# Optimization experiments

Hardware: AMD Instinct MI355X
Metric: run time of the kernel (lower is better)

## Reference

```python
import jax, jax.numpy as jnp
import numpy as np

N, E, G = 50000, 400000, 64          # nodes, edges, graphs in batch
IN_DIM, OUT_DIM = 64, 128
N_ETYPES, N_STEPS = 4, 8


def setup_inputs() -> dict:
    key = jax.random.key(0)
    ks = jax.random.split(key, 13)
    s = 1.0 / np.sqrt(OUT_DIM)
    u = lambda k, shp: jax.random.uniform(k, shp, jnp.float32, -s, s)
    return {
        "node_features": jax.random.normal(ks[0], (N, IN_DIM), jnp.float32),
        "src": jax.random.randint(ks[1], (E,), 0, N),
        "dst": jax.random.randint(ks[2], (E,), 0, N),
        "etype": jax.random.randint(ks[3], (E,), 0, N_ETYPES),
        "graph_ids": jax.random.randint(ks[4], (N,), 0, G),
        "Ws": u(ks[5], (N_ETYPES, OUT_DIM, OUT_DIM)),   # per-edge-type linear
        "bs": u(ks[6], (N_ETYPES, OUT_DIM)),
        "W_ih": u(ks[7], (3 * OUT_DIM, OUT_DIM)),        # GRUCell (r,z,n order)
        "W_hh": u(ks[8], (3 * OUT_DIM, OUT_DIM)),
        "b_ih": u(ks[9], (3 * OUT_DIM,)),
        "b_hh": u(ks[10], (3 * OUT_DIM,)),
        "W_cls": u(ks[11], (1, OUT_DIM + IN_DIM)),
        "b_cls": u(ks[12], (1,)),
    }


def _gru_cell(x, h, W_ih, W_hh, b_ih, b_hh):
    gi = x @ W_ih.T + b_ih
    gh = h @ W_hh.T + b_hh
    ir, iz, i_n = jnp.split(gi, 3, axis=-1)
    hr, hz, h_n = jnp.split(gh, 3, axis=-1)
    r = jax.nn.sigmoid(ir + hr)
    z = jax.nn.sigmoid(iz + hz)
    n = jnp.tanh(i_n + r * h_n)
    return (1.0 - z) * n + z * h


def reference(node_features, src, dst, etype, graph_ids,
              Ws, bs, W_ih, W_hh, b_ih, b_hh, W_cls, b_cls):
    # pad input features to OUT_DIM (GGNN.forward zero_pad)
    h = jnp.concatenate(
        [node_features, jnp.zeros((N, OUT_DIM - IN_DIM), node_features.dtype)], -1)

    def step(h, _):
        # per-edge-type linear transform of all node states: (T, N, D)
        Wh = jnp.einsum('nd,tkd->tnk', h, Ws) + bs[:, None, :]
        msg = Wh[etype, src]                                  # (E, D) gather
        a = jax.ops.segment_sum(msg, dst, num_segments=N)     # scatter-add
        return _gru_cell(a, h, W_ih, W_hh, b_ih, b_hh), None

    h, _ = jax.lax.scan(step, h, None, length=N_STEPS)

    hcat = jnp.concatenate([h, node_features], -1)            # (N, OUT+IN)
    feats = jax.ops.segment_sum(hcat, graph_ids, num_segments=G)  # sum readout
    return jax.nn.sigmoid(feats @ W_cls.T + b_cls)            # (G, 1)
```

## Files before the change

### kernel.cpp

```cpp
#include <hip/hip_runtime.h>
#include <hip/hip_bf16.h>
#include <math.h>


#define NN 50000
#define NE 400000
#define NG 64
#define IND 64
#define OD 128
#define NN4 (NN * 4)
#define LDO 768
#define RC 8

typedef _Float16 f16x8 __attribute__((ext_vector_type(8)));
typedef _Float16 f16x4 __attribute__((ext_vector_type(4)));
typedef _Float16 f16x2 __attribute__((ext_vector_type(2)));
typedef float f32x4 __attribute__((ext_vector_type(4)));

__device__ inline unsigned short f2h(float x) {
    _Float16 hv = (_Float16)x;
    unsigned short u;
    __builtin_memcpy(&u, &hv, 2);
    return u;
}

__global__ void k_cvt(const float* __restrict__ s, unsigned short* __restrict__ d, int n) {
    int i = blockIdx.x * 256 + threadIdx.x;
    if (i < n) d[i] = f2h(s[i]);
}

__global__ void k_init_h(const float* __restrict__ nf, float* __restrict__ h,
                         unsigned short* __restrict__ hb) {
    int i = blockIdx.x * 256 + threadIdx.x;
    if (i >= NN * OD) return;
    int n = i >> 7, d = i & 127;
    float v = (d < IND) ? nf[n * IND + d] : 0.f;
    h[i] = v;
    hb[i] = f2h(v);
}

__global__ void k_count(const int* __restrict__ dst, const int* __restrict__ et,
                        int* __restrict__ deg4) {
    int e = blockIdx.x * 256 + threadIdx.x;
    if (e < NE) atomicAdd(&deg4[dst[e] * 4 + et[e]], 1);
}

__global__ void k_scan1(const int* __restrict__ deg, int* __restrict__ rowp,
                        int* __restrict__ bsum, int n) {
    __shared__ int buf[1024];
    int tid = threadIdx.x;
    int i = blockIdx.x * 1024 + tid;
    int v = (i < n) ? deg[i] : 0;
    buf[tid] = v;
    __syncthreads();
    for (int off = 1; off < 1024; off <<= 1) {
        int t = (tid >= off) ? buf[tid - off] : 0;
        __syncthreads();
        buf[tid] += t;
        __syncthreads();
    }
    if (i < n) rowp[i + 1] = buf[tid];
    if (tid == 1023) bsum[blockIdx.x] = buf[tid];
}

__global__ void k_scan2(int* __restrict__ bsum, int nb) {
    __shared__ int buf[256];
    int tid = threadIdx.x;
    int v = (tid < nb) ? bsum[tid] : 0;
    buf[tid] = v;
    __syncthreads();
    for (int off = 1; off < 256; off <<= 1) {
        int t = (tid >= off) ? buf[tid - off] : 0;
        __syncthreads();
        buf[tid] += t;
        __syncthreads();
    }
    if (tid < nb) bsum[tid] = buf[tid] - v;
}

__global__ void k_scan3(const int* __restrict__ deg, const int* __restrict__ bsum,
                        int* __restrict__ rowp, int* __restrict__ cursor, int n) {
    int i = blockIdx.x * 256 + threadIdx.x;
    if (i >= n) return;
    int incl = rowp[i + 1] + bsum[i >> 10];
    rowp[i + 1] = incl;
    cursor[i] = incl - deg[i];
    if (i == 0) rowp[0] = 0;
}

__global__ void k_fill(const int* __restrict__ src, const int* __restrict__ dst,
                       const int* __restrict__ et, int* __restrict__ cursor,
                       int* __restrict__ esrc) {
    int e = blockIdx.x * 256 + threadIdx.x;
    if (e < NE) {
        int pos = atomicAdd(&cursor[dst[e] * 4 + et[e]], 1);
        esrc[pos] = src[e];
    }
}

__global__ void k_gcount(const int* __restrict__ gid, int* __restrict__ gdeg) {
    __shared__ int c[NG];
    int tid = threadIdx.x;
    if (tid < NG) c[tid] = 0;
    __syncthreads();
    int n = blockIdx.x * 1024 + tid;
    if (n < NN) atomicAdd(&c[gid[n]], 1);
    __syncthreads();
    if (tid < NG && c[tid] > 0) atomicAdd(&gdeg[tid], c[tid]);
}

__global__ void k_gscan(const int* __restrict__ gdeg, int* __restrict__ growp,
                        int* __restrict__ gcur) {
    __shared__ int buf[NG];
    int tid = threadIdx.x;
    int v = gdeg[tid];
    buf[tid] = v;
    __syncthreads();
    for (int off = 1; off < NG; off <<= 1) {
        int t = (tid >= off) ? buf[tid - off] : 0;
        __syncthreads();
        buf[tid] += t;
        __syncthreads();
    }
    growp[tid + 1] = buf[tid];
    gcur[tid] = buf[tid] - v;
    if (tid == 0) growp[0] = 0;
}

__global__ void k_gfill(const int* __restrict__ gid, int* __restrict__ gcur,
                        int* __restrict__ nlist) {
    __shared__ int lcnt[NG];
    __shared__ int lbase[NG];
    int tid = threadIdx.x;
    if (tid < NG) lcnt[tid] = 0;
    __syncthreads();
    int n = blockIdx.x * 1024 + tid;
    int g = -1, rank = 0;
    if (n < NN) { g = gid[n]; rank = atomicAdd(&lcnt[g], 1); }
    __syncthreads();
    if (tid < NG && lcnt[tid] > 0) lbase[tid] = atomicAdd(&gcur[tid], lcnt[tid]);
    __syncthreads();
    if (n < NN) nlist[lbase[g] + rank] = n;
}

__global__ __launch_bounds__(256) void k_agg_gemm(
    const unsigned short* __restrict__ hb,
    const int* __restrict__ rowp4, const int* __restrict__ esrc,
    const int* __restrict__ deg4,
    const unsigned short* __restrict__ Wsb,
    const float* __restrict__ bs,
    unsigned short* __restrict__ ab) {
    __shared__ unsigned short Ss[128 * 136];
    __shared__ float Bsb[512];

    const int tid = threadIdx.x;
    const int m0 = blockIdx.x * 128;

    Bsb[tid] = bs[tid];
    Bsb[tid + 256] = bs[tid + 256];

    const int r = tid >> 1;
    const int hsel = tid & 1;
    const int n = m0 + r;

    const int lane = tid & 63;
    const int w = tid >> 6;
    const int lr = lane & 15;
    const int q = lane >> 4;

    f32x4 acc[2][8];
#pragma unroll
    for (int mt = 0; mt < 2; ++mt)
#pragma unroll
        for (int nt = 0; nt < 8; ++nt) acc[mt][nt] = (f32x4){0.f, 0.f, 0.f, 0.f};

    for (int t = 0; t < 4; ++t) {
        float sacc[64];
#pragma unroll
        for (int j = 0; j < 64; ++j) sacc[j] = 0.f;
        if (n < NN) {
            int beg = rowp4[n * 4 + t], end = rowp4[n * 4 + t + 1];
            for (int i = beg; i < end; ++i) {
                const f16x8* row8 = (const f16x8*)&hb[(size_t)esrc[i] * 128 + hsel * 64];
#pragma unroll
                for (int jj = 0; jj < 8; ++jj) {
                    f16x8 v = row8[jj];
#pragma unroll
                    for (int k = 0; k < 8; ++k) sacc[jj * 8 + k] += (float)v[k];
                }
            }
        }
        __syncthreads();
#pragma unroll
        for (int jj = 0; jj < 8; ++jj) {
            f16x8 hv;
#pragma unroll
            for (int k = 0; k < 8; ++k) hv[k] = (_Float16)sacc[jj * 8 + k];
            *(f16x8*)&Ss[r * 136 + hsel * 64 + jj * 8] = hv;
        }
        __syncthreads();

        const unsigned short* Wt = Wsb + t * 16384;
#pragma unroll
        for (int ks = 0; ks < 4; ++ks) {
            f16x8 af[2];
#pragma unroll
            for (int mt = 0; mt < 2; ++mt)
                af[mt] = *(const f16x8*)&Ss[(w * 32 + mt * 16 + lr) * 136 + ks * 32 + q * 8];
#pragma unroll
            for (int nt = 0; nt < 8; ++nt) {
                f16x8 bf = *(const f16x8*)&Wt[(nt * 16 + lr) * 128 + ks * 32 + q * 8];
#pragma unroll
                for (int mt = 0; mt < 2; ++mt)
                    acc[mt][nt] = __builtin_amdgcn_mfma_f32_16x16x32_f16(
                        af[mt], bf, acc[mt][nt], 0, 0, 0);
            }
        }
    }

#pragma unroll
    for (int mt = 0; mt < 2; ++mt) {
        int rowbase = m0 + w * 32 + mt * 16 + q * 4;
#pragma unroll
        for (int rr = 0; rr < 4; ++rr) {
            int n2 = rowbase + rr;
            if (n2 < NN) {
                int4 c = *(const int4*)&deg4[n2 * 4];
                unsigned short* arow = ab + (size_t)n2 * 128;
#pragma unroll
                for (int nt = 0; nt < 8; ++nt) {
                    int col = nt * 16 + lr;
                    float v = acc[mt][nt][rr]
                            + c.x * Bsb[col] + c.y * Bsb[128 + col]
                            + c.z * Bsb[256 + col] + c.w * Bsb[384 + col];
                    arow[col] = f2h(v);
                }
            }
        }
    }
}

__global__ __launch_bounds__(256) void k_gates_gemm(
    const unsigned short* __restrict__ Aab, const unsigned short* __restrict__ Ahb,
    int M,
    const unsigned short* __restrict__ Wih, const unsigned short* __restrict__ Whh,
    const float* __restrict__ bih, const float* __restrict__ bhh,
    unsigned short* __restrict__ C) {
    __shared__ unsigned short As[128 * 136];
    __shared__ unsigned short Bs[128 * 136];

    const int g = blockIdx.y;
    const unsigned short* Ab = (g < 3) ? Aab : Ahb;
    const unsigned short* W  = (g < 3) ? (Wih + (size_t)g * 16384)
                                       : (Whh + (size_t)(g - 3) * 16384);
    const float* bias = (g < 3) ? (bih + g * 128) : (bhh + (g - 3) * 128);
    const int colbase = g * 128;
    const int m0 = blockIdx.x * 128;
    const int tid = threadIdx.x;

    const uint4* A4 = (const uint4*)Ab;
    const uint4* W4 = (const uint4*)W;

#pragma unroll
    for (int i = tid; i < 2048; i += 256) {
        int row = i >> 4, qq = i & 15;
        int nn = m0 + row;
        uint4 va = (nn < M) ? A4[(size_t)nn * 16 + qq] : make_uint4(0u, 0u, 0u, 0u);
        *(uint4*)&As[row * 136 + qq * 8] = va;
        *(uint4*)&Bs[row * 136 + qq * 8] = W4[(size_t)row * 16 + qq];
    }
    __syncthreads();

    const int lane = tid & 63;
    const int w = tid >> 6;
    const int lr = lane & 15;
    const int q = lane >> 4;

    float bv[8];
#pragma unroll
    for (int nt = 0; nt < 8; ++nt) bv[nt] = bias[nt * 16 + lr];

    f32x4 acc[2][8];
#pragma unroll
    for (int mt = 0; mt < 2; ++mt)
#pragma unroll
        for (int nt = 0; nt < 8; ++nt) acc[mt][nt] = (f32x4){0.f, 0.f, 0.f, 0.f};

#pragma unroll
    for (int ks = 0; ks < 4; ++ks) {
        f16x8 af[2];
#pragma unroll
        for (int mt = 0; mt < 2; ++mt)
            af[mt] = *(const f16x8*)&As[(w * 32 + mt * 16 + lr) * 136 + ks * 32 + q * 8];
        f16x8 bfr[8];
#pragma unroll
        for (int nt = 0; nt < 8; ++nt)
            bfr[nt] = *(const f16x8*)&Bs[(nt * 16 + lr) * 136 + ks * 32 + q * 8];
#pragma unroll
        for (int mt = 0; mt < 2; ++mt)
#pragma unroll
            for (int nt = 0; nt < 8; ++nt)
                acc[mt][nt] = __builtin_amdgcn_mfma_f32_16x16x32_f16(
                    af[mt], bfr[nt], acc[mt][nt], 0, 0, 0);
    }

#pragma unroll
    for (int mt = 0; mt < 2; ++mt) {
        int rowbase = m0 + w * 32 + mt * 16 + q * 4;
#pragma unroll
        for (int rr = 0; rr < 4; ++rr) {
            int nn = rowbase + rr;
            if (nn < M) {
                unsigned short* crow = C + (size_t)nn * LDO + colbase;
#pragma unroll
                for (int nt = 0; nt < 8; ++nt)
                    crow[nt * 16 + lr] = f2h(acc[mt][nt][rr] + bv[nt]);
            }
        }
    }
}

__global__ void k_gru(const unsigned short* __restrict__ O, float* __restrict__ h,
                      unsigned short* __restrict__ hb) {
    int i = blockIdx.x * 256 + threadIdx.x;
    if (i >= NN * 64) return;
    int n = i >> 6, p = (i & 63) * 2;
    const unsigned short* r = O + (size_t)n * LDO;
    f16x2 ir = *(const f16x2*)&r[p];
    f16x2 iz = *(const f16x2*)&r[128 + p];
    f16x2 in_ = *(const f16x2*)&r[256 + p];
    f16x2 hr = *(const f16x2*)&r[384 + p];
    f16x2 hz = *(const f16x2*)&r[512 + p];
    f16x2 hn = *(const f16x2*)&r[640 + p];
    float2 hv = *(const float2*)&h[(size_t)n * OD + p];
    float2 nh;
    {
        float rg = 1.f / (1.f + __expf(-((float)ir[0] + (float)hr[0])));
        float zg = 1.f / (1.f + __expf(-((float)iz[0] + (float)hz[0])));
        float ng = tanhf((float)in_[0] + rg * (float)hn[0]);
        nh.x = (1.f - zg) * ng + zg * hv.x;
        rg = 1.f / (1.f + __expf(-((float)ir[1] + (float)hr[1])));
        zg = 1.f / (1.f + __expf(-((float)iz[1] + (float)hz[1])));
        ng = tanhf((float)in_[1] + rg * (float)hn[1]);
        nh.y = (1.f - zg) * ng + zg * hv.y;
    }
    *(float2*)&h[(size_t)n * OD + p] = nh;
    f16x2 hb2; hb2[0] = (_Float16)nh.x; hb2[1] = (_Float16)nh.y;
    *(f16x2*)&hb[(size_t)n * OD + p] = hb2;
}

__global__ void k_readout(const float* __restrict__ h, const float* __restrict__ nf,
                          const int* __restrict__ nlist, const int* __restrict__ growp,
                          float* __restrict__ partial) {
    int g = blockIdx.x >> 3, c = blockIdx.x & (RC - 1);
    int d = threadIdx.x;
    int s = growp[g], e = growp[g + 1], len = e - s;
    int i0 = s + (int)((long long)len * c / RC);
    int i1 = s + (int)((long long)len * (c + 1) / RC);
    float acc = 0.f;
    for (int i = i0; i < i1; ++i) {
        int n = nlist[i];
        acc += (d < OD) ? h[(size_t)n * OD + d] : nf[(size_t)n * IND + (d - OD)];
    }
    partial[(size_t)blockIdx.x * 192 + d] = acc;
}

__global__ void k_reduce(const float* __restrict__ partial, float* __restrict__ feats) {
    int i = blockIdx.x * 256 + threadIdx.x;
    if (i >= NG * 192) return;
    int g = i / 192, d = i % 192;
    float s = 0.f;
    for (int c = 0; c < RC; ++c) s += partial[(size_t)(g * RC + c) * 192 + d];
    feats[i] = s;
}

__global__ void k_final(const float* __restrict__ feats, const float* __restrict__ W_cls,
                        const float* __restrict__ b_cls, float* __restrict__ out) {
    int g = threadIdx.x;
    if (g >= NG) return;
    float acc = b_cls[0];
    for (int d = 0; d < 192; ++d) acc += feats[g * 192 + d] * W_cls[d];
    out[g] = 1.f / (1.f + __expf(-acc));
}

extern "C" void kernel_launch(void* const* d_in, const int* in_sizes, int n_in,
                              void* d_out, int out_size, void* d_ws, size_t ws_size,
                              hipStream_t stream) {
    const float* nf    = (const float*)d_in[0];
    const int*   src   = (const int*)d_in[1];
    const int*   dst   = (const int*)d_in[2];
    const int*   et    = (const int*)d_in[3];
    const int*   gid   = (const int*)d_in[4];
    const float* Ws    = (const float*)d_in[5];
    const float* bs    = (const float*)d_in[6];
    const float* W_ih  = (const float*)d_in[7];
    const float* W_hh  = (const float*)d_in[8];
    const float* b_ih  = (const float*)d_in[9];
    const float* b_hh  = (const float*)d_in[10];
    const float* W_cls = (const float*)d_in[11];
    const float* b_cls = (const float*)d_in[12];
    float* out = (float*)d_out;

    char* ws = (char*)d_ws;
    size_t off = 0;
    auto alloc = [&](size_t bytes) -> void* {
        off = (off + 255) & ~(size_t)255;
        void* p = ws + off;
        off += bytes;
        return p;
    };
    float*          h    = (float*)alloc((size_t)NN * OD * 4);
    unsigned short* O    = (unsigned short*)alloc((size_t)NN * LDO * 2);
    unsigned short* hb   = (unsigned short*)alloc((size_t)NN * OD * 2);
    unsigned short* ab   = (unsigned short*)alloc((size_t)NN * OD * 2);
    int*   deg4    = (int*)alloc((size_t)NN4 * 4);
    int*   rowp4   = (int*)alloc((size_t)(NN4 + 1) * 4);
    int*   cursor4 = (int*)alloc((size_t)NN4 * 4);
    int*   esrc    = (int*)alloc((size_t)NE * 4);
    int*   bsum    = (int*)alloc(256 * 4);
    int*   gdeg    = (int*)alloc(NG * 4);
    int*   growp   = (int*)alloc((NG + 1) * 4);
    int*   gcur    = (int*)alloc(NG * 4);
    int*   nlist   = (int*)alloc((size_t)NN * 4);
    float* feats   = (float*)alloc((size_t)NG * 192 * 4);
    unsigned short* wsb  = (unsigned short*)alloc((size_t)4 * 16384 * 2);
    unsigned short* wihb = (unsigned short*)alloc((size_t)3 * 16384 * 2);
    unsigned short* whhb = (unsigned short*)alloc((size_t)3 * 16384 * 2);
    (void)ws_size; (void)in_sizes; (void)n_in; (void)out_size;

    float* partial = (float*)O;

    hipMemsetAsync(deg4, 0, (size_t)NN4 * 4, stream);
    hipMemsetAsync(gdeg, 0, NG * 4, stream);

    k_cvt<<<(4 * 16384 + 255) / 256, 256, 0, stream>>>(Ws, wsb, 4 * 16384);
    k_cvt<<<(3 * 16384 + 255) / 256, 256, 0, stream>>>(W_ih, wihb, 3 * 16384);
    k_cvt<<<(3 * 16384 + 255) / 256, 256, 0, stream>>>(W_hh, whhb, 3 * 16384);

    k_init_h<<<(NN * OD + 255) / 256, 256, 0, stream>>>(nf, h, hb);

    k_count<<<(NE + 255) / 256, 256, 0, stream>>>(dst, et, deg4);
    const int nb4 = (NN4 + 1023) / 1024;
    k_scan1<<<nb4, 1024, 0, stream>>>(deg4, rowp4, bsum, NN4);
    k_scan2<<<1, 256, 0, stream>>>(bsum, nb4);
    k_scan3<<<(NN4 + 255) / 256, 256, 0, stream>>>(deg4, bsum, rowp4, cursor4, NN4);
    k_fill<<<(NE + 255) / 256, 256, 0, stream>>>(src, dst, et, cursor4, esrc);

    const int nbn = (NN + 1023) / 1024;
    k_gcount<<<nbn, 1024, 0, stream>>>(gid, gdeg);
    k_gscan<<<1, NG, 0, stream>>>(gdeg, growp, gcur);
    k_gfill<<<nbn, 1024, 0, stream>>>(gid, gcur, nlist);

    const int mt = (NN + 127) / 128;
    for (int s = 0; s < 8; ++s) {
        k_agg_gemm<<<mt, 256, 0, stream>>>(hb, rowp4, esrc, deg4, wsb, bs, ab);
        k_gates_gemm<<<dim3(mt, 6), 256, 0, stream>>>(ab, hb, NN, wihb, whhb,
                                                      b_ih, b_hh, O);
        k_gru<<<(NN * 64 + 255) / 256, 256, 0, stream>>>(O, h, hb);
    }

    k_readout<<<NG * RC, 192, 0, stream>>>(h, nf, nlist, growp, partial);
    k_reduce<<<(NG * 192 + 255) / 256, 256, 0, stream>>>(partial, feats);
    k_final<<<1, 64, 0, stream>>>(feats, W_cls, b_cls, out);
}
```

Baseline: 1.165 ms.

## Fuse gate GEMMs with GRU update and interleave a/h into one buffer

```diff
diff --git a/kernel.cpp b/kernel.cpp
--- a/kernel.cpp
+++ b/kernel.cpp
@@ -9,7 +9,6 @@
 #define IND 64
 #define OD 128
 #define NN4 (NN * 4)
-#define LDO 768
 #define RC 8
 
 typedef _Float16 f16x8 __attribute__((ext_vector_type(8)));
@@ -29,14 +28,37 @@
     if (i < n) d[i] = f2h(s[i]);
 }
 
+__global__ void k_pack(const float* __restrict__ Wih, const float* __restrict__ Whh,
+                       const float* __restrict__ bih, const float* __restrict__ bhh,
+                       unsigned short* __restrict__ Wpk, float* __restrict__ bpk) {
+    int i = blockIdx.x * 256 + threadIdx.x;
+    if (i < 65536) {
+        int o = i >> 8, k = i & 255;
+        float v = (k < 128) ? Wih[o * 128 + k] : Whh[o * 128 + (k - 128)];
+        Wpk[i] = f2h(v);
+    } else if (i < 98304) {
+        int j = i - 65536;
+        int o = j >> 7, k = j & 127;
+        float v = (o < 128) ? Wih[(256 + o) * 128 + k] : Whh[(256 + (o - 128)) * 128 + k];
+        Wpk[i] = f2h(v);
+    }
+    if (i < 512) {
+        float b;
+        if (i < 256) b = bih[i] + bhh[i];
+        else if (i < 384) b = bih[i];
+        else b = bhh[i - 128];
+        bpk[i] = b;
+    }
+}
+
 __global__ void k_init_h(const float* __restrict__ nf, float* __restrict__ h,
-                         unsigned short* __restrict__ hb) {
+                         unsigned short* __restrict__ hx) {
     int i = blockIdx.x * 256 + threadIdx.x;
     if (i >= NN * OD) return;
     int n = i >> 7, d = i & 127;
     float v = (d < IND) ? nf[n * IND + d] : 0.f;
     h[i] = v;
-    hb[i] = f2h(v);
+    hx[(size_t)n * 256 + 128 + d] = f2h(v);
 }
 
 __global__ void k_count(const int* __restrict__ dst, const int* __restrict__ et,
@@ -144,23 +166,23 @@
 }
 
 __global__ __launch_bounds__(256) void k_agg_gemm(
-    const unsigned short* __restrict__ hb,
+    const unsigned short* __restrict__ hx,
     const int* __restrict__ rowp4, const int* __restrict__ esrc,
     const int* __restrict__ deg4,
     const unsigned short* __restrict__ Wsb,
     const float* __restrict__ bs,
-    unsigned short* __restrict__ ab) {
-    __shared__ unsigned short Ss[128 * 136];
+    unsigned short* __restrict__ hxw) {
+    __shared__ unsigned short Ss[64 * 136];
     __shared__ float Bsb[512];
 
     const int tid = threadIdx.x;
-    const int m0 = blockIdx.x * 128;
+    const int m0 = blockIdx.x * 64;
 
     Bsb[tid] = bs[tid];
     Bsb[tid + 256] = bs[tid + 256];
 
-    const int r = tid >> 1;
-    const int hsel = tid & 1;
+    const int r = tid >> 2;
+    const int hsel = tid & 3;
     const int n = m0 + r;
 
     const int lane = tid & 63;
@@ -168,22 +190,21 @@
     const int lr = lane & 15;
     const int q = lane >> 4;
 
-    f32x4 acc[2][8];
-#pragma unroll
-    for (int mt = 0; mt < 2; ++mt)
-#pragma unroll
-        for (int nt = 0; nt < 8; ++nt) acc[mt][nt] = (f32x4){0.f, 0.f, 0.f, 0.f};
+    f32x4 acc[8];
+#pragma unroll
+    for (int nt = 0; nt < 8; ++nt) acc[nt] = (f32x4){0.f, 0.f, 0.f, 0.f};
 
     for (int t = 0; t < 4; ++t) {
-        float sacc[64];
-#pragma unroll
-        for (int j = 0; j < 64; ++j) sacc[j] = 0.f;
+        float sacc[32];
+#pragma unroll
+        for (int j = 0; j < 32; ++j) sacc[j] = 0.f;
         if (n < NN) {
             int beg = rowp4[n * 4 + t], end = rowp4[n * 4 + t + 1];
             for (int i = beg; i < end; ++i) {
-                const f16x8* row8 = (const f16x8*)&hb[(size_t)esrc[i] * 128 + hsel * 64];
-#pragma unroll
-                for (int jj = 0; jj < 8; ++jj) {
+                const f16x8* row8 =
+                    (const f16x8*)&hx[(size_t)esrc[i] * 256 + 128 + hsel * 32];
+#pragma unroll
+                for (int jj = 0; jj < 4; ++jj) {
                     f16x8 v = row8[jj];
 #pragma unroll
                     for (int k = 0; k < 8; ++k) sacc[jj * 8 + k] += (float)v[k];
@@ -192,82 +213,68 @@
         }
         __syncthreads();
 #pragma unroll
-        for (int jj = 0; jj < 8; ++jj) {
+        for (int jj = 0; jj < 4; ++jj) {
             f16x8 hv;
 #pragma unroll
             for (int k = 0; k < 8; ++k) hv[k] = (_Float16)sacc[jj * 8 + k];
-            *(f16x8*)&Ss[r * 136 + hsel * 64 + jj * 8] = hv;
+            *(f16x8*)&Ss[r * 136 + hsel * 32 + jj * 8] = hv;
         }
         __syncthreads();
 
         const unsigned short* Wt = Wsb + t * 16384;
 #pragma unroll
         for (int ks = 0; ks < 4; ++ks) {
-            f16x8 af[2];
-#pragma unroll
-            for (int mt = 0; mt < 2; ++mt)
-                af[mt] = *(const f16x8*)&Ss[(w * 32 + mt * 16 + lr) * 136 + ks * 32 + q * 8];
+            f16x8 af = *(const f16x8*)&Ss[(w * 16 + lr) * 136 + ks * 32 + q * 8];
 #pragma unroll
             for (int nt = 0; nt < 8; ++nt) {
                 f16x8 bf = *(const f16x8*)&Wt[(nt * 16 + lr) * 128 + ks * 32 + q * 8];
-#pragma unroll
-                for (int mt = 0; mt < 2; ++mt)
-                    acc[mt][nt] = __builtin_amdgcn_mfma_f32_16x16x32_f16(
-                        af[mt], bf, acc[mt][nt], 0, 0, 0);
+                acc[nt] = __builtin_amdgcn_mfma_f32_16x16x32_f16(af, bf, acc[nt], 0, 0, 0);
             }
         }
     }
 
-#pragma unroll
-    for (int mt = 0; mt < 2; ++mt) {
-        int rowbase = m0 + w * 32 + mt * 16 + q * 4;
-#pragma unroll
-        for (int rr = 0; rr < 4; ++rr) {
-            int n2 = rowbase + rr;
-            if (n2 < NN) {
-                int4 c = *(const int4*)&deg4[n2 * 4];
-                unsigned short* arow = ab + (size_t)n2 * 128;
-#pragma unroll
-                for (int nt = 0; nt < 8; ++nt) {
-                    int col = nt * 16 + lr;
-                    float v = acc[mt][nt][rr]
-                            + c.x * Bsb[col] + c.y * Bsb[128 + col]
-                            + c.z * Bsb[256 + col] + c.w * Bsb[384 + col];
-                    arow[col] = f2h(v);
-                }
+    int rowbase = m0 + w * 16 + q * 4;
+#pragma unroll
+    for (int rr = 0; rr < 4; ++rr) {
+        int n2 = rowbase + rr;
+        if (n2 < NN) {
+            int4 c = *(const int4*)&deg4[n2 * 4];
+            unsigned short* arow = hxw + (size_t)n2 * 256;
+#pragma unroll
+            for (int nt = 0; nt < 8; ++nt) {
+                int col = nt * 16 + lr;
+                float v = acc[nt][rr]
+                        + c.x * Bsb[col] + c.y * Bsb[128 + col]
+                        + c.z * Bsb[256 + col] + c.w * Bsb[384 + col];
+                arow[col] = f2h(v);
             }
         }
     }
 }
 
-__global__ __launch_bounds__(256) void k_gates_gemm(
-    const unsigned short* __restrict__ Aab, const unsigned short* __restrict__ Ahb,
-    int M,
-    const unsigned short* __restrict__ Wih, const unsigned short* __restrict__ Whh,
-    const float* __restrict__ bih, const float* __restrict__ bhh,
-    unsigned short* __restrict__ C) {
-    __shared__ unsigned short As[128 * 136];
-    __shared__ unsigned short Bs[128 * 136];
-
-    const int g = blockIdx.y;
-    const unsigned short* Ab = (g < 3) ? Aab : Ahb;
-    const unsigned short* W  = (g < 3) ? (Wih + (size_t)g * 16384)
-                                       : (Whh + (size_t)(g - 3) * 16384);
-    const float* bias = (g < 3) ? (bih + g * 128) : (bhh + (g - 3) * 128);
-    const int colbase = g * 128;
-    const int m0 = blockIdx.x * 128;
+__global__ __launch_bounds__(256) void k_gates_gru(
+    const unsigned short* __restrict__ hx,
+    const unsigned short* __restrict__ Wpk,
+    const float* __restrict__ bpk,
+    float* __restrict__ h,
+    unsigned short* __restrict__ hxw) {
+    __shared__ unsigned short As[2 * 64 * 136];
+    __shared__ float Bsb[512];
+
     const int tid = threadIdx.x;
-
-    const uint4* A4 = (const uint4*)Ab;
-    const uint4* W4 = (const uint4*)W;
-
-#pragma unroll
-    for (int i = tid; i < 2048; i += 256) {
-        int row = i >> 4, qq = i & 15;
+    const int m0 = blockIdx.x * 64;
+
+    Bsb[tid] = bpk[tid];
+    Bsb[tid + 256] = bpk[tid + 256];
+
+    const uint4* H4 = (const uint4*)hx;
+#pragma unroll
+    for (int it = 0; it < 8; ++it) {
+        int i = tid + it * 256;
+        int row = i >> 5, qq = i & 31;
         int nn = m0 + row;
-        uint4 va = (nn < M) ? A4[(size_t)nn * 16 + qq] : make_uint4(0u, 0u, 0u, 0u);
-        *(uint4*)&As[row * 136 + qq * 8] = va;
-        *(uint4*)&Bs[row * 136 + qq * 8] = W4[(size_t)row * 16 + qq];
+        uint4 v = (nn < NN) ? H4[(size_t)nn * 32 + qq] : make_uint4(0u, 0u, 0u, 0u);
+        *(uint4*)&As[(qq >> 4) * 8704 + row * 136 + (qq & 15) * 8] = v;
     }
     __syncthreads();
 
@@ -276,77 +283,64 @@
     const int lr = lane & 15;
     const int q = lane >> 4;
 
-    float bv[8];
-#pragma unroll
-    for (int nt = 0; nt < 8; ++nt) bv[nt] = bias[nt * 16 + lr];
-
-    f32x4 acc[2][8];
-#pragma unroll
-    for (int mt = 0; mt < 2; ++mt)
-#pragma unroll
-        for (int nt = 0; nt < 8; ++nt) acc[mt][nt] = (f32x4){0.f, 0.f, 0.f, 0.f};
+    f32x4 acc[32];
+#pragma unroll
+    for (int j = 0; j < 32; ++j) acc[j] = (f32x4){0.f, 0.f, 0.f, 0.f};
+
+    const int arow = (w * 16 + lr) * 136;
+    const int brow = nullptr == nullptr ? 0 : 0;
+    (void)brow;
 
 #pragma unroll
     for (int ks = 0; ks < 4; ++ks) {
-        f16x8 af[2];
-#pragma unroll
-        for (int mt = 0; mt < 2; ++mt)
-            af[mt] = *(const f16x8*)&As[(w * 32 + mt * 16 + lr) * 136 + ks * 32 + q * 8];
-        f16x8 bfr[8];
-#pragma unroll
-        for (int nt = 0; nt < 8; ++nt)
-            bfr[nt] = *(const f16x8*)&Bs[(nt * 16 + lr) * 136 + ks * 32 + q * 8];
-#pragma unroll
-        for (int mt = 0; mt < 2; ++mt)
-#pragma unroll
-            for (int nt = 0; nt < 8; ++nt)
-                acc[mt][nt] = __builtin_amdgcn_mfma_f32_16x16x32_f16(
-                    af[mt], bfr[nt], acc[mt][nt], 0, 0, 0);
-    }
-
-#pragma unroll
-    for (int mt = 0; mt < 2; ++mt) {
-        int rowbase = m0 + w * 32 + mt * 16 + q * 4;
-#pragma unroll
-        for (int rr = 0; rr < 4; ++rr) {
-            int nn = rowbase + rr;
-            if (nn < M) {
-                unsigned short* crow = C + (size_t)nn * LDO + colbase;
-#pragma unroll
-                for (int nt = 0; nt < 8; ++nt)
-                    crow[nt * 16 + lr] = f2h(acc[mt][nt][rr] + bv[nt]);
+        f16x8 af = *(const f16x8*)&As[arow + ks * 32 + q * 8];
+#pragma unroll
+        for (int nt = 0; nt < 8; ++nt) {
+            int wr = (nt * 16 + lr);
+            f16x8 bfR = *(const f16x8*)&Wpk[wr * 256 + ks * 32 + q * 8];
+            acc[nt] = __builtin_amdgcn_mfma_f32_16x16x32_f16(af, bfR, acc[nt], 0, 0, 0);
+            f16x8 bfZ = *(const f16x8*)&Wpk[32768 + wr * 256 + ks * 32 + q * 8];
+            acc[8 + nt] = __builtin_amdgcn_mfma_f32_16x16x32_f16(af, bfZ, acc[8 + nt], 0, 0, 0);
+            f16x8 bfI = *(const f16x8*)&Wpk[65536 + wr * 128 + ks * 32 + q * 8];
+            acc[16 + nt] = __builtin_amdgcn_mfma_f32_16x16x32_f16(af, bfI, acc[16 + nt], 0, 0, 0);
+        }
+    }
+#pragma unroll
+    for (int ks = 4; ks < 8; ++ks) {
+        f16x8 af = *(const f16x8*)&As[8704 + arow + (ks - 4) * 32 + q * 8];
+#pragma unroll
+        for (int nt = 0; nt < 8; ++nt) {
+            int wr = (nt * 16 + lr);
+            f16x8 bfR = *(const f16x8*)&Wpk[wr * 256 + ks * 32 + q * 8];
+            acc[nt] = __builtin_amdgcn_mfma_f32_16x16x32_f16(af, bfR, acc[nt], 0, 0, 0);
+            f16x8 bfZ = *(const f16x8*)&Wpk[32768 + wr * 256 + ks * 32 + q * 8];
+            acc[8 + nt] = __builtin_amdgcn_mfma_f32_16x16x32_f16(af, bfZ, acc[8 + nt], 0, 0, 0);
+            f16x8 bfH = *(const f16x8*)&Wpk[81920 + wr * 128 + (ks - 4) * 32 + q * 8];
+            acc[24 + nt] = __builtin_amdgcn_mfma_f32_16x16x32_f16(af, bfH, acc[24 + nt], 0, 0, 0);
+        }
+    }
+
+    int rowbase = m0 + w * 16 + q * 4;
+#pragma unroll
+    for (int rr = 0; rr < 4; ++rr) {
+        int n2 = rowbase + rr;
+        if (n2 < NN) {
+            float* hrow = h + (size_t)n2 * OD;
+            unsigned short* hxrow = hxw + (size_t)n2 * 256 + 128;
+#pragma unroll
+            for (int nt = 0; nt < 8; ++nt) {
+                int col = nt * 16 + lr;
+                float R = 1.f / (1.f + __expf(-(acc[nt][rr] + Bsb[col])));
+                float Z = 1.f / (1.f + __expf(-(acc[8 + nt][rr] + Bsb[128 + col])));
+                float NV = tanhf(acc[16 + nt][rr] + Bsb[256 + col]
+                                 + R * (acc[24 + nt][rr] + Bsb[384 + col]));
+                float hold = hrow[col];
+                float hnew = (1.f - Z) * NV + Z * hold;
+                hrow[col] = hnew;
+                hxrow[col] = f2h(hnew);
             }
         }
     }
-}
-
-__global__ void k_gru(const unsigned short* __restrict__ O, float* __restrict__ h,
-                      unsigned short* __restrict__ hb) {
-    int i = blockIdx.x * 256 + threadIdx.x;
-    if (i >= NN * 64) return;
-    int n = i >> 6, p = (i & 63) * 2;
-    const unsigned short* r = O + (size_t)n * LDO;
-    f16x2 ir = *(const f16x2*)&r[p];
-    f16x2 iz = *(const f16x2*)&r[128 + p];
-    f16x2 in_ = *(const f16x2*)&r[256 + p];
-    f16x2 hr = *(const f16x2*)&r[384 + p];
-    f16x2 hz = *(const f16x2*)&r[512 + p];
-    f16x2 hn = *(const f16x2*)&r[640 + p];
-    float2 hv = *(const float2*)&h[(size_t)n * OD + p];
-    float2 nh;
-    {
-        float rg = 1.f / (1.f + __expf(-((float)ir[0] + (float)hr[0])));
-        float zg = 1.f / (1.f + __expf(-((float)iz[0] + (float)hz[0])));
-        float ng = tanhf((float)in_[0] + rg * (float)hn[0]);
-        nh.x = (1.f - zg) * ng + zg * hv.x;
-        rg = 1.f / (1.f + __expf(-((float)ir[1] + (float)hr[1])));
-        zg = 1.f / (1.f + __expf(-((float)iz[1] + (float)hz[1])));
-        ng = tanhf((float)in_[1] + rg * (float)hn[1]);
-        nh.y = (1.f - zg) * ng + zg * hv.y;
-    }
-    *(float2*)&h[(size_t)n * OD + p] = nh;
-    f16x2 hb2; hb2[0] = (_Float16)nh.x; hb2[1] = (_Float16)nh.y;
-    *(f16x2*)&hb[(size_t)n * OD + p] = hb2;
 }
 
 __global__ void k_readout(const float* __restrict__ h, const float* __restrict__ nf,
@@ -410,9 +404,7 @@
         return p;
     };
     float*          h    = (float*)alloc((size_t)NN * OD * 4);
-    unsigned short* O    = (unsigned short*)alloc((size_t)NN * LDO * 2);
-    unsigned short* hb   = (unsigned short*)alloc((size_t)NN * OD * 2);
-    unsigned short* ab   = (unsigned short*)alloc((size_t)NN * OD * 2);
+    unsigned short* hx   = (unsigned short*)alloc((size_t)NN * 256 * 2);
     int*   deg4    = (int*)alloc((size_t)NN4 * 4);
     int*   rowp4   = (int*)alloc((size_t)(NN4 + 1) * 4);
     int*   cursor4 = (int*)alloc((size_t)NN4 * 4);
@@ -423,21 +415,19 @@
     int*   gcur    = (int*)alloc(NG * 4);
     int*   nlist   = (int*)alloc((size_t)NN * 4);
     float* feats   = (float*)alloc((size_t)NG * 192 * 4);
-    unsigned short* wsb  = (unsigned short*)alloc((size_t)4 * 16384 * 2);
-    unsigned short* wihb = (unsigned short*)alloc((size_t)3 * 16384 * 2);
-    unsigned short* whhb = (unsigned short*)alloc((size_t)3 * 16384 * 2);
+    float* partial = (float*)alloc((size_t)NG * RC * 192 * 4);
+    unsigned short* wsb = (unsigned short*)alloc((size_t)4 * 16384 * 2);
+    unsigned short* Wpk = (unsigned short*)alloc((size_t)98304 * 2);
+    float*          bpk = (float*)alloc(512 * 4);
     (void)ws_size; (void)in_sizes; (void)n_in; (void)out_size;
-
-    float* partial = (float*)O;
 
     hipMemsetAsync(deg4, 0, (size_t)NN4 * 4, stream);
     hipMemsetAsync(gdeg, 0, NG * 4, stream);
 
     k_cvt<<<(4 * 16384 + 255) / 256, 256, 0, stream>>>(Ws, wsb, 4 * 16384);
-    k_cvt<<<(3 * 16384 + 255) / 256, 256, 0, stream>>>(W_ih, wihb, 3 * 16384);
-    k_cvt<<<(3 * 16384 + 255) / 256, 256, 0, stream>>>(W_hh, whhb, 3 * 16384);
-
-    k_init_h<<<(NN * OD + 255) / 256, 256, 0, stream>>>(nf, h, hb);
+    k_pack<<<(98304 + 255) / 256, 256, 0, stream>>>(W_ih, W_hh, b_ih, b_hh, Wpk, bpk);
+
+    k_init_h<<<(NN * OD + 255) / 256, 256, 0, stream>>>(nf, h, hx);
 
     k_count<<<(NE + 255) / 256, 256, 0, stream>>>(dst, et, deg4);
     const int nb4 = (NN4 + 1023) / 1024;
@@ -451,12 +441,10 @@
     k_gscan<<<1, NG, 0, stream>>>(gdeg, growp, gcur);
     k_gfill<<<nbn, 1024, 0, stream>>>(gid, gcur, nlist);
 
-    const int mt = (NN + 127) / 128;
+    const int mt64 = (NN + 63) / 64;
     for (int s = 0; s < 8; ++s) {
-        k_agg_gemm<<<mt, 256, 0, stream>>>(hb, rowp4, esrc, deg4, wsb, bs, ab);
-        k_gates_gemm<<<dim3(mt, 6), 256, 0, stream>>>(ab, hb, NN, wihb, whhb,
-                                                      b_ih, b_hh, O);
-        k_gru<<<(NN * 64 + 255) / 256, 256, 0, stream>>>(O, h, hb);
+        k_agg_gemm<<<mt64, 256, 0, stream>>>(hx, rowp4, esrc, deg4, wsb, bs, hx);
+        k_gates_gru<<<mt64, 256, 0, stream>>>(hx, Wpk, bpk, h, hx);
     }
 
     k_readout<<<NG * RC, 192, 0, stream>>>(h, nf, nlist, growp, partial);
```

New measurement: 2.044 ms. 1.75x slower.
